# Optimization experiments

Hardware: AMD Instinct MI355X
Metric: run time of the kernel (lower is better)

The kernel has to match this reference:

```python
import jax, jax.numpy as jnp
import numpy as np

B, H, W, K = 256, 28, 28, 5

def grid_edges_np(nb, h, w):
    # directed 8-neighbor edges on an h x w grid, replicated for nb graphs
    idx = np.arange(h * w).reshape(h, w)
    src_l, dst_l = [], []
    for dy in (-1, 0, 1):
        for dx in (-1, 0, 1):
            if dy == 0 and dx == 0:
                continue
            s = idx[max(0, -dy):h - max(0, dy), max(0, -dx):w - max(0, dx)]
            d = idx[max(0, dy):h - max(0, -dy), max(0, dx):w - max(0, -dx)]
            src_l.append(s.ravel()); dst_l.append(d.ravel())
    e = np.stack([np.concatenate(src_l), np.concatenate(dst_l)])
    off = np.arange(nb) * h * w
    return (e[:, None, :] + off[None, :, None]).reshape(2, -1).astype(np.int32)

def cart_pseudo(pos, src, dst):
    # CartesianAdj: relative offsets normalized into [0,1]^2
    cart = pos[dst] - pos[src]
    return cart / (2.0 * jnp.max(jnp.abs(cart))) + 0.5

def spline_conv(x, src, dst, pseudo, Wk, root, bias):
    # SplineConv, dim=2, kernel_size=K, degree-1 open B-splines, mean aggregation
    n = x.shape[0]
    v = jnp.clip(pseudo, 0.0, 1.0) * (K - 1)
    i0 = jnp.clip(jnp.floor(v), 0, K - 1).astype(jnp.int32)
    frac = v - i0.astype(v.dtype)
    i1 = jnp.minimum(i0 + 1, K - 1)
    Y = jnp.einsum('nf,kfg->nkg', x, Wk)  # [N, K*K, Fout]
    msg = 0.0
    for ia, ba in ((i0[:, 0], 1.0 - frac[:, 0]), (i1[:, 0], frac[:, 0])):
        for jb, bb in ((i0[:, 1], 1.0 - frac[:, 1]), (i1[:, 1], frac[:, 1])):
            msg = msg + (ba * bb)[:, None] * Y[src, ia * K + jb]
    cnt = jax.ops.segment_sum(jnp.ones((src.shape[0],), x.dtype), dst, num_segments=n)
    agg = jax.ops.segment_sum(msg, dst, num_segments=n) / jnp.maximum(cnt, 1.0)[:, None]
    return agg + x @ root + bias

def voxel_pool(x, pos, size, gy, gx, npi):
    # voxel-grid clustering: max-pool features, mean-pool positions
    batch = jnp.repeat(jnp.arange(B), npi)
    c = jnp.floor(pos / size).astype(jnp.int32)
    c = jnp.clip(c, 0, jnp.array([gx - 1, gy - 1], dtype=jnp.int32))
    cid = batch * (gy * gx) + c[:, 1] * gx + c[:, 0]
    ns = B * gy * gx
    xp = jax.ops.segment_max(x, cid, num_segments=ns)
    cnt = jax.ops.segment_sum(jnp.ones((x.shape[0],), x.dtype), cid, num_segments=ns)
    pp = jax.ops.segment_sum(pos, cid, num_segments=ns) / cnt[:, None]
    return xp, pp

def setup_inputs():
    key = jax.random.key(0)
    ks = jax.random.split(key, 10)
    ei = grid_edges_np(B, H, W)
    yy, xx = np.meshgrid(np.arange(H), np.arange(W), indexing='ij')
    p = np.stack([xx.ravel(), yy.ravel()], 1).astype(np.float32)
    pos = np.tile(p, (B, 1))
    cart = pos[ei[1]] - pos[ei[0]]
    pseudo = (cart / (2.0 * np.abs(cart).max()) + 0.5).astype(np.float32)
    r = lambda k, s, sc: jax.random.normal(k, s, dtype=jnp.float32) * sc
    return {
        'x': jax.random.normal(ks[0], (B * H * W, 1), dtype=jnp.float32),
        'pos': jnp.asarray(pos), 'pseudo': jnp.asarray(pseudo),
        'W1': r(ks[1], (K * K, 1, 32), 0.3), 'root1': r(ks[2], (1, 32), 0.3), 'b1': jnp.zeros((32,), jnp.float32),
        'W2': r(ks[3], (K * K, 32, 64), 0.08), 'root2': r(ks[4], (32, 64), 0.08), 'b2': jnp.zeros((64,), jnp.float32),
        'W3': r(ks[5], (K * K, 64, 64), 0.06), 'root3': r(ks[6], (64, 64), 0.06), 'b3': jnp.zeros((64,), jnp.float32),
        'fc1_w': r(ks[7], (256, 128), 0.06), 'fc1_b': jnp.zeros((128,), jnp.float32),
        'fc2_w': r(ks[8], (128, 10), 0.09), 'fc2_b': jnp.zeros((10,), jnp.float32),
        'edge_index': jnp.asarray(ei),
    }

def reference(x, pos, pseudo, W1, root1, b1, W2, root2, b2, W3, root3, b3, fc1_w, fc1_b, fc2_w, fc2_b, edge_index):
    src, dst = edge_index[0], edge_index[1]
    h = jax.nn.elu(spline_conv(x, src, dst, pseudo, W1, root1, b1))
    h, pos1 = voxel_pool(h, pos, 5.0, 6, 6, H * W)            # 28x28 -> 6x6
    e1 = jnp.asarray(grid_edges_np(B, 6, 6))
    h = jax.nn.elu(spline_conv(h, e1[0], e1[1], cart_pseudo(pos1, e1[0], e1[1]), W2, root2, b2))
    h, pos2 = voxel_pool(h, pos1, 7.0, 4, 4, 36)              # 6x6 -> 4x4
    e2 = jnp.asarray(grid_edges_np(B, 4, 4))
    h = jax.nn.elu(spline_conv(h, e2[0], e2[1], cart_pseudo(pos2, e2[0], e2[1]), W3, root3, b3))
    h, _ = voxel_pool(h, pos2, 14.0, 2, 2, 16)                # dense pool -> 2x2 = 4 clusters
    h = h.reshape(B, 4 * 64)
    h = jax.nn.elu(h @ fc1_w + fc1_b)
    # dropout is identity in eval mode
    h = h @ fc2_w + fc2_b
    return jax.nn.log_softmax(h, axis=1)
```

## Files before the change

kernel.cpp:

```cpp
#include <hip/hip_runtime.h>
#include <hip/hip_bf16.h>
#include <math.h>


#define DEV __device__ __forceinline__

DEV float elu_f(float v) { return v > 0.f ? v : expm1f(v); }

DEV void corners(float p0, float p1,
                 int& k00, int& k01, int& k10, int& k11,
                 float& w00, float& w01, float& w10, float& w11) {
  float v0 = fminf(fmaxf(p0, 0.f), 1.f) * 4.f;
  float v1 = fminf(fmaxf(p1, 0.f), 1.f) * 4.f;
  int i0 = (int)v0; i0 = i0 > 4 ? 4 : i0;
  int j0 = (int)v1; j0 = j0 > 4 ? 4 : j0;
  float f0 = v0 - (float)i0;
  float f1 = v1 - (float)j0;
  int i1 = i0 + 1 > 4 ? 4 : i0 + 1;
  int j1 = j0 + 1 > 4 ? 4 : j0 + 1;
  k00 = i0 * 5 + j0; k01 = i0 * 5 + j1; k10 = i1 * 5 + j0; k11 = i1 * 5 + j1;
  w00 = (1.f - f0) * (1.f - f1); w01 = (1.f - f0) * f1;
  w10 = f0 * (1.f - f1);         w11 = f0 * f1;
}

DEV float cellpos(int c, int gw) {
  return (gw == 6) ? (c < 5 ? 2.f + 5.f * (float)c : 26.f)
                   : (c < 3 ? 2.f + 7.5f * (float)c : 24.f);
}

__constant__ int c_dys[8] = {-1, -1, -1, 0, 0, 1, 1, 1};
__constant__ int c_dxs[8] = {-1, 0, 1, -1, 1, -1, 0, 1};

__global__ __launch_bounds__(256) void s1p1_kernel(
    const float* __restrict__ xin, const float* __restrict__ W1,
    const float* __restrict__ root1, const float* __restrict__ b1,
    float* __restrict__ h1p) {
  int id = blockIdx.x * 256 + threadIdx.x;
  int g = id & 31, cell = id >> 5;
  int b = cell / 36, r = cell % 36;
  int cy = r / 6, cx = r % 6;
  int y0 = cy * 5, y1 = y0 + 5 > 28 ? 28 : y0 + 5;
  int x0 = cx * 5, x1 = x0 + 5 > 28 ? 28 : x0 + 5;
  float Wreg[8];
#pragma unroll
  for (int d = 0; d < 8; d++) {
    int k = (2 * c_dxs[d] + 2) * 5 + (2 * c_dys[d] + 2);
    Wreg[d] = W1[k * 32 + g];
  }
  float rt = root1[g], bs = b1[g];
  const float* xb = xin + b * 784;
  float vmax = -3.4e38f;
  for (int y = y0; y < y1; y++) {
    for (int x = x0; x < x1; x++) {
      float acc = 0.f;
#pragma unroll
      for (int d = 0; d < 8; d++) {
        int sy = y - c_dys[d], sx = x - c_dxs[d];
        if (sy >= 0 && sy < 28 && sx >= 0 && sx < 28)
          acc += xb[sy * 28 + sx] * Wreg[d];
      }
      float cnt = (float)((1 + (y > 0) + (y < 27)) * (1 + (x > 0) + (x < 27)) - 1);
      float v = acc * (1.f / cnt) + xb[y * 28 + x] * rt + bs;
      vmax = fmaxf(vmax, elu_f(v));
    }
  }
  h1p[cell * 32 + g] = vmax;
}

__global__ __launch_bounds__(256) void prepM_kernel(
    const float* __restrict__ W2, const float* __restrict__ root2,
    const float* __restrict__ W3, const float* __restrict__ root3,
    float* __restrict__ M2, float* __restrict__ M3) {
  int idx = blockIdx.x * 256 + threadIdx.x;
  const int L2N = 36 * 9 * 32 * 64;
  int gw, F, c, d, f, g;
  const float *W, *root;
  float inv2M;
  float* Mout;
  int oidx;
  if (idx < L2N) {
    c = idx / 18432; int rem = idx % 18432;
    d = rem / 2048; f = (rem >> 6) & 31; g = rem & 63;
    gw = 6; F = 32; W = W2; root = root2; inv2M = 0.1f; Mout = M2; oidx = idx;
  } else {
    int j = idx - L2N;
    c = j / 36864; int rem = j % 36864;
    d = rem / 4096; f = (rem >> 6) & 63; g = rem & 63;
    gw = 4; F = 64; W = W3; root = root3; inv2M = 1.f / 15.f; Mout = M3; oidx = j;
  }
  float val = 0.f;
  if (d == 8) {
    val = root[f * 64 + g];
  } else {
    int cy = c / gw, cx = c % gw;
    int sy = cy - c_dys[d], sx = cx - c_dxs[d];
    if (sy >= 0 && sy < gw && sx >= 0 && sx < gw) {
      int cnt = (1 + (cy > 0) + (cy < gw - 1)) * (1 + (cx > 0) + (cx < gw - 1)) - 1;
      float invc = 1.f / (float)cnt;
      float p0 = (cellpos(cx, gw) - cellpos(sx, gw)) * inv2M + 0.5f;
      float p1 = (cellpos(cy, gw) - cellpos(sy, gw)) * inv2M + 0.5f;
      int k00, k01, k10, k11; float w00, w01, w10, w11;
      corners(p0, p1, k00, k01, k10, k11, w00, w01, w10, w11);
      val = invc * (w00 * W[(k00 * F + f) * 64 + g] + w01 * W[(k01 * F + f) * 64 + g] +
                    w10 * W[(k10 * F + f) * 64 + g] + w11 * W[(k11 * F + f) * 64 + g]);
    }
  }
  Mout[oidx] = val;
}

__global__ __launch_bounds__(256) void gemm_cls_kernel(
    const float* __restrict__ X, const float* __restrict__ M,
    float* __restrict__ P, int per, int fshift, int NC, int dps, int gw) {
  __shared__ float At[16][64];
  __shared__ float Bt[16][64];
  __shared__ int nbL[9];
  int t = threadIdx.x;
  int b0 = blockIdx.x * 64, c = blockIdx.y, s = blockIdx.z;
  int F = 1 << fshift, fmask = F - 1;
  if (t < 9) {
    int cy = c / gw, cx = c % gw;
    int nb = c;
    if (t < 8) {
      int sy = cy - c_dys[t], sx = cx - c_dxs[t];
      nb = (sy >= 0 && sy < gw && sx >= 0 && sx < gw) ? sy * gw + sx : c;
    }
    nbL[t] = nb;
  }
  __syncthreads();

  int tx = t & 15, ty = t >> 4;
  int kqA = (t & 3) * 4, rA = t >> 2;
  int bkB = t >> 4, bnB = (t & 15) * 4;
  float acc[4][4];
#pragma unroll
  for (int i = 0; i < 4; i++)
#pragma unroll
    for (int j = 0; j < 4; j++) acc[i][j] = 0.f;

  int chunkK = dps << fshift;
  for (int k0 = 0; k0 < chunkK; k0 += 16) {
    int kA = k0 + kqA;
    int dA = s * dps + (kA >> fshift);
    int fA = kA & fmask;
    float4 xv = *(const float4*)&X[(((b0 + rA) * per + nbL[dA]) << fshift) + fA];
    int kB = k0 + bkB;
    int dB = s * dps + (kB >> fshift);
    int fB = kB & fmask;
    float4 bv = *(const float4*)&M[(size_t)(((c * 9 + dB) << fshift) + fB) * 64 + bnB];
    __syncthreads();
    At[kqA + 0][rA] = xv.x; At[kqA + 1][rA] = xv.y;
    At[kqA + 2][rA] = xv.z; At[kqA + 3][rA] = xv.w;
    *(float4*)&Bt[bkB][bnB] = bv;
    __syncthreads();
#pragma unroll
    for (int kk = 0; kk < 16; kk++) {
      float4 a = *(const float4*)&At[kk][ty * 4];
      float4 bb = *(const float4*)&Bt[kk][tx * 4];
      acc[0][0] += a.x * bb.x; acc[0][1] += a.x * bb.y; acc[0][2] += a.x * bb.z; acc[0][3] += a.x * bb.w;
      acc[1][0] += a.y * bb.x; acc[1][1] += a.y * bb.y; acc[1][2] += a.y * bb.z; acc[1][3] += a.y * bb.w;
      acc[2][0] += a.z * bb.x; acc[2][1] += a.z * bb.y; acc[2][2] += a.z * bb.z; acc[2][3] += a.z * bb.w;
      acc[3][0] += a.w * bb.x; acc[3][1] += a.w * bb.y; acc[3][2] += a.w * bb.z; acc[3][3] += a.w * bb.w;
    }
  }
  float* Pq = P + ((size_t)(s * NC + c) * 256 + b0) * 64;
#pragma unroll
  for (int i = 0; i < 4; i++) {
    float4 v = {acc[i][0], acc[i][1], acc[i][2], acc[i][3]};
    *(float4*)&Pq[(size_t)(ty * 4 + i) * 64 + tx * 4] = v;
  }
}

__global__ __launch_bounds__(256) void redpool2_kernel(
    const float* __restrict__ P, const float* __restrict__ bias,
    float* __restrict__ h2p) {
  int id = blockIdx.x * 256 + threadIdx.x;
  int g = id & 63, s2 = id >> 6;
  int b = s2 >> 4, r = s2 & 15;
  int oy = r >> 2, ox = r & 3;
  int ys = oy == 0 ? 0 : (oy == 1 ? 1 : (oy == 2 ? 3 : 4));
  int yn = (oy == 1 || oy == 3) ? 2 : 1;
  int xs = ox == 0 ? 0 : (ox == 1 ? 1 : (ox == 2 ? 3 : 4));
  int xn = (ox == 1 || ox == 3) ? 2 : 1;
  float bg = bias[g];
  const size_t CS = (size_t)36 * 256 * 64;
  float vmax = -3.4e38f;
  for (int yy = ys; yy < ys + yn; yy++)
    for (int xx = xs; xx < xs + xn; xx++) {
      size_t e = (size_t)((yy * 6 + xx) * 256 + b) * 64 + g;
      float v = P[e] + P[CS + e] + P[2 * CS + e] + bg;
      vmax = fmaxf(vmax, elu_f(v));
    }
  h2p[(size_t)s2 * 64 + g] = vmax;
}

__global__ __launch_bounds__(256) void redpool3_kernel(
    const float* __restrict__ P, const float* __restrict__ bias,
    float* __restrict__ h3p) {
  int id = blockIdx.x * 256 + threadIdx.x;
  int g = id & 63, s2 = id >> 6;
  int b = s2 >> 2, r = s2 & 3;
  int oy = r >> 1, ox = r & 1;
  float bg = bias[g];
  const size_t CS = (size_t)16 * 256 * 64;
  float vmax = -3.4e38f;
#pragma unroll
  for (int i = 0; i < 2; i++)
#pragma unroll
    for (int j = 0; j < 2; j++) {
      int cy = oy * 2 + i, cx = ox * 2 + j;
      size_t e = (size_t)((cy * 4 + cx) * 256 + b) * 64 + g;
      float v = bg;
#pragma unroll
      for (int q = 0; q < 9; q++) v += P[q * CS + e];
      vmax = fmaxf(vmax, elu_f(v));
    }
  h3p[(size_t)s2 * 64 + g] = vmax;
}

__global__ __launch_bounds__(128) void fc_head_kernel(
    const float* __restrict__ h3p, const float* __restrict__ fc1w,
    const float* __restrict__ fc1b, const float* __restrict__ fc2w,
    const float* __restrict__ fc2b, float* __restrict__ out) {
  __shared__ float Al[256];
  __shared__ float h4l[128];
  __shared__ float lg[10];
  int b = blockIdx.x, t = threadIdx.x;
  Al[t] = h3p[b * 256 + t];
  Al[t + 128] = h3p[b * 256 + 128 + t];
  __syncthreads();
  float acc = fc1b[t];
  for (int k = 0; k < 256; k++) acc += Al[k] * fc1w[k * 128 + t];
  h4l[t] = elu_f(acc);
  __syncthreads();
  if (t < 10) {
    float l = fc2b[t];
    for (int k = 0; k < 128; k++) l += h4l[k] * fc2w[k * 10 + t];
    lg[t] = l;
  }
  __syncthreads();
  if (t < 10) {
    float m = lg[0];
#pragma unroll
    for (int j = 1; j < 10; j++) m = fmaxf(m, lg[j]);
    float ssum = 0.f;
#pragma unroll
    for (int j = 0; j < 10; j++) ssum += expf(lg[j] - m);
    out[b * 10 + t] = lg[t] - m - logf(ssum);
  }
}

extern "C" void kernel_launch(void* const* d_in, const int* in_sizes, int n_in,
                              void* d_out, int out_size, void* d_ws, size_t ws_size,
                              hipStream_t stream) {
  const float* x     = (const float*)d_in[0];
  const float* W1    = (const float*)d_in[3];
  const float* root1 = (const float*)d_in[4];
  const float* b1    = (const float*)d_in[5];
  const float* W2    = (const float*)d_in[6];
  const float* root2 = (const float*)d_in[7];
  const float* b2    = (const float*)d_in[8];
  const float* W3    = (const float*)d_in[9];
  const float* root3 = (const float*)d_in[10];
  const float* b3    = (const float*)d_in[11];
  const float* fc1w  = (const float*)d_in[12];
  const float* fc1b  = (const float*)d_in[13];
  const float* fc2w  = (const float*)d_in[14];
  const float* fc2b  = (const float*)d_in[15];
  float* out = (float*)d_out;

  float* ws = (float*)d_ws;
  size_t o = 0;
  float* w_h1p = ws + o; o += (size_t)9216 * 32;
  float* w_M2  = ws + o; o += (size_t)36 * 9 * 32 * 64;
  float* w_M3  = ws + o; o += (size_t)16 * 9 * 64 * 64;
  float* w_P   = ws + o; o += (size_t)9 * 16 * 256 * 64;
  float* w_h2p = ws + o; o += (size_t)4096 * 64;
  float* w_h3p = ws + o; o += (size_t)1024 * 64;

  s1p1_kernel<<<1152, 256, 0, stream>>>(x, W1, root1, b1, w_h1p);
  prepM_kernel<<<4896, 256, 0, stream>>>(W2, root2, W3, root3, w_M2, w_M3);
  gemm_cls_kernel<<<dim3(4, 36, 3), 256, 0, stream>>>(w_h1p, w_M2, w_P, 36, 5, 36, 3, 6);
  redpool2_kernel<<<1024, 256, 0, stream>>>(w_P, b2, w_h2p);
  gemm_cls_kernel<<<dim3(4, 16, 9), 256, 0, stream>>>(w_h2p, w_M3, w_P, 16, 6, 16, 1, 4);
  redpool3_kernel<<<256, 256, 0, stream>>>(w_P, b3, w_h3p);
  fc_head_kernel<<<256, 128, 0, stream>>>(w_h3p, fc1w, fc1b, fc2w, fc2b, out);
}
```

Before: 176.0 us.

## Fuse whole network into one cooperative persistent kernel with grid syncs

Replaces the chain of seven kernel launches with one cooperative persistent kernel. Each stage runs as a grid-stride loop over virtual blocks, with grid.sync between stages, to remove launch gaps and per-kernel tail effects. The layer-3 reduce, pool and FC head are fused into one body, the fc1 dot product is split across 256 threads, and the GEMM parameters become template constants. The persistent grid is capped at 512 blocks, so stages with more blocks run serially. The grid-wide barriers add sync overhead in exchange.

```diff
diff --git a/kernel.cpp b/kernel.cpp
--- a/kernel.cpp
+++ b/kernel.cpp
@@ -1,6 +1,8 @@
 #include <hip/hip_runtime.h>
-#include <hip/hip_bf16.h>
+#include <hip/hip_cooperative_groups.h>
 #include <math.h>
+
+namespace cg = cooperative_groups;
 
 
 #define DEV __device__ __forceinline__
@@ -31,11 +33,16 @@
 __constant__ int c_dys[8] = {-1, -1, -1, 0, 0, 1, 1, 1};
 __constant__ int c_dxs[8] = {-1, 0, 1, -1, 1, -1, 0, 1};
 
-__global__ __launch_bounds__(256) void s1p1_kernel(
-    const float* __restrict__ xin, const float* __restrict__ W1,
-    const float* __restrict__ root1, const float* __restrict__ b1,
-    float* __restrict__ h1p) {
-  int id = blockIdx.x * 256 + threadIdx.x;
+union SMem {
+  struct { float At[16][64]; float Bt[16][64]; int nbL[9]; } g;
+  struct { float h3[16][64]; float Al[256]; float part[256];
+           float h4[128]; float lg[10]; } f;
+};
+
+
+DEV void s1p1_body(int id, const float* __restrict__ xin,
+                   const float* __restrict__ W1, const float* __restrict__ root1,
+                   const float* __restrict__ b1, float* __restrict__ h1p) {
   int g = id & 31, cell = id >> 5;
   int b = cell / 36, r = cell % 36;
   int cy = r / 6, cx = r % 6;
@@ -67,11 +74,10 @@
   h1p[cell * 32 + g] = vmax;
 }
 
-__global__ __launch_bounds__(256) void prepM_kernel(
-    const float* __restrict__ W2, const float* __restrict__ root2,
-    const float* __restrict__ W3, const float* __restrict__ root3,
-    float* __restrict__ M2, float* __restrict__ M3) {
-  int idx = blockIdx.x * 256 + threadIdx.x;
+DEV void prepM_body(int idx, const float* __restrict__ W2,
+                    const float* __restrict__ root2, const float* __restrict__ W3,
+                    const float* __restrict__ root3, float* __restrict__ M2,
+                    float* __restrict__ M3) {
   const int L2N = 36 * 9 * 32 * 64;
   int gw, F, c, d, f, g;
   const float *W, *root;
@@ -108,23 +114,22 @@
   Mout[oidx] = val;
 }
 
-__global__ __launch_bounds__(256) void gemm_cls_kernel(
-    const float* __restrict__ X, const float* __restrict__ M,
-    float* __restrict__ P, int per, int fshift, int NC, int dps, int gw) {
-  __shared__ float At[16][64];
-  __shared__ float Bt[16][64];
-  __shared__ int nbL[9];
-  int t = threadIdx.x;
-  int b0 = blockIdx.x * 64, c = blockIdx.y, s = blockIdx.z;
-  int F = 1 << fshift, fmask = F - 1;
+template <int PER, int FSHIFT, int NC, int DPS, int GW>
+DEV void gemm_body(int vb, int t, SMem* sm, const float* __restrict__ X,
+                   const float* __restrict__ M, float* __restrict__ P) {
+  int s = vb / (4 * NC);
+  int rem = vb - s * 4 * NC;
+  int c = rem >> 2;
+  int b0 = (rem & 3) * 64;
+  constexpr int F = 1 << FSHIFT, fmask = F - 1;
   if (t < 9) {
-    int cy = c / gw, cx = c % gw;
-    int nb = c;
+    int cy = c / GW, cx = c % GW;
+    int nbv = c;
     if (t < 8) {
       int sy = cy - c_dys[t], sx = cx - c_dxs[t];
-      nb = (sy >= 0 && sy < gw && sx >= 0 && sx < gw) ? sy * gw + sx : c;
-    }
-    nbL[t] = nb;
+      nbv = (sy >= 0 && sy < GW && sx >= 0 && sx < GW) ? sy * GW + sx : c;
+    }
+    sm->g.nbL[t] = nbv;
   }
   __syncthreads();
 
@@ -137,25 +142,25 @@
 #pragma unroll
     for (int j = 0; j < 4; j++) acc[i][j] = 0.f;
 
-  int chunkK = dps << fshift;
+  constexpr int chunkK = DPS << FSHIFT;
   for (int k0 = 0; k0 < chunkK; k0 += 16) {
     int kA = k0 + kqA;
-    int dA = s * dps + (kA >> fshift);
+    int dA = s * DPS + (kA >> FSHIFT);
     int fA = kA & fmask;
-    float4 xv = *(const float4*)&X[(((b0 + rA) * per + nbL[dA]) << fshift) + fA];
+    float4 xv = *(const float4*)&X[(((b0 + rA) * PER + sm->g.nbL[dA]) << FSHIFT) + fA];
     int kB = k0 + bkB;
-    int dB = s * dps + (kB >> fshift);
+    int dB = s * DPS + (kB >> FSHIFT);
     int fB = kB & fmask;
-    float4 bv = *(const float4*)&M[(size_t)(((c * 9 + dB) << fshift) + fB) * 64 + bnB];
+    float4 bv = *(const float4*)&M[(size_t)(((c * 9 + dB) << FSHIFT) + fB) * 64 + bnB];
     __syncthreads();
-    At[kqA + 0][rA] = xv.x; At[kqA + 1][rA] = xv.y;
-    At[kqA + 2][rA] = xv.z; At[kqA + 3][rA] = xv.w;
-    *(float4*)&Bt[bkB][bnB] = bv;
+    sm->g.At[kqA + 0][rA] = xv.x; sm->g.At[kqA + 1][rA] = xv.y;
+    sm->g.At[kqA + 2][rA] = xv.z; sm->g.At[kqA + 3][rA] = xv.w;
+    *(float4*)&sm->g.Bt[bkB][bnB] = bv;
     __syncthreads();
 #pragma unroll
     for (int kk = 0; kk < 16; kk++) {
-      float4 a = *(const float4*)&At[kk][ty * 4];
-      float4 bb = *(const float4*)&Bt[kk][tx * 4];
+      float4 a = *(const float4*)&sm->g.At[kk][ty * 4];
+      float4 bb = *(const float4*)&sm->g.Bt[kk][tx * 4];
       acc[0][0] += a.x * bb.x; acc[0][1] += a.x * bb.y; acc[0][2] += a.x * bb.z; acc[0][3] += a.x * bb.w;
       acc[1][0] += a.y * bb.x; acc[1][1] += a.y * bb.y; acc[1][2] += a.y * bb.z; acc[1][3] += a.y * bb.w;
       acc[2][0] += a.z * bb.x; acc[2][1] += a.z * bb.y; acc[2][2] += a.z * bb.z; acc[2][3] += a.z * bb.w;
@@ -170,10 +175,8 @@
   }
 }
 
-__global__ __launch_bounds__(256) void redpool2_kernel(
-    const float* __restrict__ P, const float* __restrict__ bias,
-    float* __restrict__ h2p) {
-  int id = blockIdx.x * 256 + threadIdx.x;
+DEV void redpool2_body(int id, const float* __restrict__ P,
+                       const float* __restrict__ bias, float* __restrict__ h2p) {
   int g = id & 63, s2 = id >> 6;
   int b = s2 >> 4, r = s2 & 15;
   int oy = r >> 2, ox = r & 3;
@@ -193,60 +196,139 @@
   h2p[(size_t)s2 * 64 + g] = vmax;
 }
 
-__global__ __launch_bounds__(256) void redpool3_kernel(
-    const float* __restrict__ P, const float* __restrict__ bias,
-    float* __restrict__ h3p) {
-  int id = blockIdx.x * 256 + threadIdx.x;
-  int g = id & 63, s2 = id >> 6;
-  int b = s2 >> 2, r = s2 & 3;
-  int oy = r >> 1, ox = r & 1;
-  float bg = bias[g];
+DEV void fc_body(int b, int t, SMem* sm, const float* __restrict__ P,
+                 const float* __restrict__ b3, const float* __restrict__ fc1w,
+                 const float* __restrict__ fc1b, const float* __restrict__ fc2w,
+                 const float* __restrict__ fc2b, float* __restrict__ out) {
   const size_t CS = (size_t)16 * 256 * 64;
-  float vmax = -3.4e38f;
-#pragma unroll
-  for (int i = 0; i < 2; i++)
-#pragma unroll
-    for (int j = 0; j < 2; j++) {
-      int cy = oy * 2 + i, cx = ox * 2 + j;
-      size_t e = (size_t)((cy * 4 + cx) * 256 + b) * 64 + g;
-      float v = bg;
-#pragma unroll
-      for (int q = 0; q < 9; q++) v += P[q * CS + e];
-      vmax = fmaxf(vmax, elu_f(v));
-    }
-  h3p[(size_t)s2 * 64 + g] = vmax;
-}
-
-__global__ __launch_bounds__(128) void fc_head_kernel(
-    const float* __restrict__ h3p, const float* __restrict__ fc1w,
-    const float* __restrict__ fc1b, const float* __restrict__ fc2w,
-    const float* __restrict__ fc2b, float* __restrict__ out) {
-  __shared__ float Al[256];
-  __shared__ float h4l[128];
-  __shared__ float lg[10];
-  int b = blockIdx.x, t = threadIdx.x;
-  Al[t] = h3p[b * 256 + t];
-  Al[t + 128] = h3p[b * 256 + 128 + t];
-  __syncthreads();
-  float acc = fc1b[t];
-  for (int k = 0; k < 256; k++) acc += Al[k] * fc1w[k * 128 + t];
-  h4l[t] = elu_f(acc);
+#pragma unroll
+  for (int i = 0; i < 4; i++) {
+    int idx = i * 256 + t;
+    int cell = idx >> 6, g = idx & 63;
+    float v = b3[g];
+    size_t e = (size_t)(cell * 256 + b) * 64 + g;
+#pragma unroll
+    for (int q = 0; q < 9; q++) v += P[q * CS + e];
+    sm->f.h3[cell][g] = elu_f(v);
+  }
+  __syncthreads();
+  {
+    int r = t >> 6, g = t & 63;
+    int oy = r >> 1, ox = r & 1;
+    float m = -3.4e38f;
+#pragma unroll
+    for (int i = 0; i < 2; i++)
+#pragma unroll
+      for (int j = 0; j < 2; j++)
+        m = fmaxf(m, sm->f.h3[(oy * 2 + i) * 4 + (ox * 2 + j)][g]);
+    sm->f.Al[t] = m;
+  }
+  __syncthreads();
+  {
+    int o = t & 127, half = t >> 7;
+    float acc = 0.f;
+    const float* wcol = fc1w + o;
+#pragma unroll 8
+    for (int k = half * 128; k < half * 128 + 128; k++)
+      acc += sm->f.Al[k] * wcol[k * 128];
+    sm->f.part[t] = acc;
+  }
+  __syncthreads();
+  if (t < 128)
+    sm->f.h4[t] = elu_f(sm->f.part[t] + sm->f.part[t + 128] + fc1b[t]);
   __syncthreads();
   if (t < 10) {
     float l = fc2b[t];
-    for (int k = 0; k < 128; k++) l += h4l[k] * fc2w[k * 10 + t];
-    lg[t] = l;
+#pragma unroll 8
+    for (int k = 0; k < 128; k++) l += sm->f.h4[k] * fc2w[k * 10 + t];
+    sm->f.lg[t] = l;
   }
   __syncthreads();
   if (t < 10) {
-    float m = lg[0];
-#pragma unroll
-    for (int j = 1; j < 10; j++) m = fmaxf(m, lg[j]);
+    float m = sm->f.lg[0];
+#pragma unroll
+    for (int j = 1; j < 10; j++) m = fmaxf(m, sm->f.lg[j]);
     float ssum = 0.f;
 #pragma unroll
-    for (int j = 0; j < 10; j++) ssum += expf(lg[j] - m);
-    out[b * 10 + t] = lg[t] - m - logf(ssum);
-  }
+    for (int j = 0; j < 10; j++) ssum += expf(sm->f.lg[j] - m);
+    out[b * 10 + t] = sm->f.lg[t] - m - logf(ssum);
+  }
+}
+
+struct NetArgs {
+  const float *x, *W1, *root1, *b1;
+  const float *W2, *root2, *b2;
+  const float *W3, *root3, *b3;
+  const float *fc1w, *fc1b, *fc2w, *fc2b;
+  float *out;
+  float *h1p, *M2, *M3, *P, *h2p;
+};
+
+__global__ __launch_bounds__(256, 2) void net_kernel(NetArgs a) {
+  __shared__ SMem sm;
+  cg::grid_group grid = cg::this_grid();
+  const int t = threadIdx.x;
+  const int nblk = gridDim.x;
+
+  for (int vb = blockIdx.x; vb < 6048; vb += nblk) {
+    if (vb < 1152) s1p1_body(vb * 256 + t, a.x, a.W1, a.root1, a.b1, a.h1p);
+    else           prepM_body((vb - 1152) * 256 + t, a.W2, a.root2, a.W3, a.root3,
+                              a.M2, a.M3);
+  }
+  __threadfence();
+  grid.sync();
+  for (int vb = blockIdx.x; vb < 432; vb += nblk)
+    gemm_body<36, 5, 36, 3, 6>(vb, t, &sm, a.h1p, a.M2, a.P);
+  __threadfence();
+  grid.sync();
+  for (int vb = blockIdx.x; vb < 1024; vb += nblk)
+    redpool2_body(vb * 256 + t, a.P, a.b2, a.h2p);
+  __threadfence();
+  grid.sync();
+  for (int vb = blockIdx.x; vb < 576; vb += nblk)
+    gemm_body<16, 6, 16, 1, 4>(vb, t, &sm, a.h2p, a.M3, a.P);
+  __threadfence();
+  grid.sync();
+  for (int vb = blockIdx.x; vb < 256; vb += nblk)
+    fc_body(vb, t, &sm, a.P, a.b3, a.fc1w, a.fc1b, a.fc2w, a.fc2b, a.out);
+}
+
+__global__ __launch_bounds__(256) void s1p1_kernel(
+    const float* __restrict__ xin, const float* __restrict__ W1,
+    const float* __restrict__ root1, const float* __restrict__ b1,
+    float* __restrict__ h1p) {
+  s1p1_body(blockIdx.x * 256 + threadIdx.x, xin, W1, root1, b1, h1p);
+}
+
+__global__ __launch_bounds__(256) void prepM_kernel(
+    const float* __restrict__ W2, const float* __restrict__ root2,
+    const float* __restrict__ W3, const float* __restrict__ root3,
+    float* __restrict__ M2, float* __restrict__ M3) {
+  prepM_body(blockIdx.x * 256 + threadIdx.x, W2, root2, W3, root3, M2, M3);
+}
+
+template <int PER, int FSHIFT, int NC, int DPS, int GW>
+__global__ __launch_bounds__(256) void gemm_cls_tk(
+    const float* __restrict__ X, const float* __restrict__ M,
+    float* __restrict__ P) {
+  __shared__ SMem sm;
+  int vb = (blockIdx.z * NC + blockIdx.y) * 4 + blockIdx.x;
+  gemm_body<PER, FSHIFT, NC, DPS, GW>(vb, threadIdx.x, &sm, X, M, P);
+}
+
+__global__ __launch_bounds__(256) void redpool2_kernel(
+    const float* __restrict__ P, const float* __restrict__ bias,
+    float* __restrict__ h2p) {
+  redpool2_body(blockIdx.x * 256 + threadIdx.x, P, bias, h2p);
+}
+
+__global__ __launch_bounds__(256) void fc_fused_kernel(
+    const float* __restrict__ P, const float* __restrict__ b3,
+    const float* __restrict__ fc1w, const float* __restrict__ fc1b,
+    const float* __restrict__ fc2w, const float* __restrict__ fc2b,
+    float* __restrict__ out) {
+  __shared__ SMem sm;
+  fc_body(blockIdx.x, threadIdx.x, &sm, P, b3, fc1w, fc1b, fc2w, fc2b, out);
 }
 
 extern "C" void kernel_launch(void* const* d_in, const int* in_sizes, int n_in,
@@ -275,13 +357,36 @@
   float* w_M3  = ws + o; o += (size_t)16 * 9 * 64 * 64;
   float* w_P   = ws + o; o += (size_t)9 * 16 * 256 * 64;
   float* w_h2p = ws + o; o += (size_t)4096 * 64;
-  float* w_h3p = ws + o; o += (size_t)1024 * 64;
-
-  s1p1_kernel<<<1152, 256, 0, stream>>>(x, W1, root1, b1, w_h1p);
-  prepM_kernel<<<4896, 256, 0, stream>>>(W2, root2, W3, root3, w_M2, w_M3);
-  gemm_cls_kernel<<<dim3(4, 36, 3), 256, 0, stream>>>(w_h1p, w_M2, w_P, 36, 5, 36, 3, 6);
-  redpool2_kernel<<<1024, 256, 0, stream>>>(w_P, b2, w_h2p);
-  gemm_cls_kernel<<<dim3(4, 16, 9), 256, 0, stream>>>(w_h2p, w_M3, w_P, 16, 6, 16, 1, 4);
-  redpool3_kernel<<<256, 256, 0, stream>>>(w_P, b3, w_h3p);
-  fc_head_kernel<<<256, 128, 0, stream>>>(w_h3p, fc1w, fc1b, fc2w, fc2b, out);
-}
+
+  NetArgs a;
+  a.x = x; a.W1 = W1; a.root1 = root1; a.b1 = b1;
+  a.W2 = W2; a.root2 = root2; a.b2 = b2;
+  a.W3 = W3; a.root3 = root3; a.b3 = b3;
+  a.fc1w = fc1w; a.fc1b = fc1b; a.fc2w = fc2w; a.fc2b = fc2b;
+  a.out = out;
+  a.h1p = w_h1p; a.M2 = w_M2; a.M3 = w_M3; a.P = w_P; a.h2p = w_h2p;
+
+  static int s_grid = 0;
+  if (s_grid == 0) {
+    int perCU = 0;
+    if (hipOccupancyMaxActiveBlocksPerMultiprocessor(
+            &perCU, (const void*)net_kernel, 256, 0) != hipSuccess || perCU <= 0)
+      perCU = 2;
+    long g = (long)perCU * 256;
+    s_grid = (int)(g < 512 ? g : 512);
+  }
+
+  void* kargs[] = { (void*)&a };
+  hipError_t err = hipLaunchCooperativeKernel((const void*)net_kernel,
+                                              dim3(s_grid), dim3(256), kargs,
+                                              0, stream);
+  if (err != hipSuccess) {
+    (void)hipGetLastError();
+    s1p1_kernel<<<1152, 256, 0, stream>>>(x, W1, root1, b1, w_h1p);
+    prepM_kernel<<<4896, 256, 0, stream>>>(W2, root2, W3, root3, w_M2, w_M3);
+    gemm_cls_tk<36, 5, 36, 3, 6><<<dim3(4, 36, 3), 256, 0, stream>>>(w_h1p, w_M2, w_P);
+    redpool2_kernel<<<1024, 256, 0, stream>>>(w_P, b2, w_h2p);
+    gemm_cls_tk<16, 6, 16, 1, 4><<<dim3(4, 16, 9), 256, 0, stream>>>(w_h2p, w_M3, w_P);
+    fc_fused_kernel<<<256, 256, 0, stream>>>(w_P, b3, fc1w, fc1b, fc2w, fc2b, out);
+  }
+}
```

Measured after the change: 493.5 us. 2.8x slower.

## Fuse pooling into GEMM epilogues via atomic max and merge prep kernels

Applied to the files above, without the earlier changes.

Merges the layer-1 conv+pool kernel, the spline weight-matrix precompute and the zeroing of the pooled buffers into one launch. The split-K GEMMs with separate reduce/pool kernels are replaced by full-K GEMMs that max-pool straight into order-preserving uint buffers with atomicMax. Bias and ELU are applied later, when the pooled value is read. This works because ELU plus a per-channel bias is monotone, so it commutes with max. It cuts launches and the large partial-sum traffic, but the GEMMs now run with far fewer blocks (144 and 128) and serial K loops, which may reduce parallelism. The FC head is also split over 256 threads.

```diff
diff --git a/kernel.cpp b/kernel.cpp
--- a/kernel.cpp
+++ b/kernel.cpp
@@ -1,11 +1,19 @@
 #include <hip/hip_runtime.h>
-#include <hip/hip_bf16.h>
 #include <math.h>
 
 
 #define DEV __device__ __forceinline__
 
 DEV float elu_f(float v) { return v > 0.f ? v : expm1f(v); }
+
+DEV unsigned int fmap(float f) {
+  unsigned int b = __float_as_uint(f);
+  return (b & 0x80000000u) ? ~b : (b | 0x80000000u);
+}
+DEV float funmap(unsigned int u) {
+  unsigned int b = (u & 0x80000000u) ? (u & 0x7fffffffu) : ~u;
+  return __uint_as_float(b);
+}
 
 DEV void corners(float p0, float p1,
                  int& k00, int& k01, int& k10, int& k11,
@@ -28,14 +36,15 @@
                    : (c < 3 ? 2.f + 7.5f * (float)c : 24.f);
 }
 
+DEV int ymap6(int c) { return c == 0 ? 0 : (c <= 2 ? 1 : (c == 3 ? 2 : 3)); }
+
 __constant__ int c_dys[8] = {-1, -1, -1, 0, 0, 1, 1, 1};
 __constant__ int c_dxs[8] = {-1, 0, 1, -1, 1, -1, 0, 1};
 
-__global__ __launch_bounds__(256) void s1p1_kernel(
-    const float* __restrict__ xin, const float* __restrict__ W1,
-    const float* __restrict__ root1, const float* __restrict__ b1,
-    float* __restrict__ h1p) {
-  int id = blockIdx.x * 256 + threadIdx.x;
+
+DEV void s1p1_body(int id, const float* __restrict__ xin,
+                   const float* __restrict__ W1, const float* __restrict__ root1,
+                   const float* __restrict__ b1, float* __restrict__ h1p) {
   int g = id & 31, cell = id >> 5;
   int b = cell / 36, r = cell % 36;
   int cy = r / 6, cx = r % 6;
@@ -67,11 +76,10 @@
   h1p[cell * 32 + g] = vmax;
 }
 
-__global__ __launch_bounds__(256) void prepM_kernel(
-    const float* __restrict__ W2, const float* __restrict__ root2,
-    const float* __restrict__ W3, const float* __restrict__ root3,
-    float* __restrict__ M2, float* __restrict__ M3) {
-  int idx = blockIdx.x * 256 + threadIdx.x;
+DEV void prepM_body(int idx, const float* __restrict__ W2,
+                    const float* __restrict__ root2, const float* __restrict__ W3,
+                    const float* __restrict__ root3, float* __restrict__ M2,
+                    float* __restrict__ M3) {
   const int L2N = 36 * 9 * 32 * 64;
   int gw, F, c, d, f, g;
   const float *W, *root;
@@ -108,23 +116,42 @@
   Mout[oidx] = val;
 }
 
-__global__ __launch_bounds__(256) void gemm_cls_kernel(
-    const float* __restrict__ X, const float* __restrict__ M,
-    float* __restrict__ P, int per, int fshift, int NC, int dps, int gw) {
+__global__ __launch_bounds__(256) void prep_kernel(
+    const float* __restrict__ x, const float* __restrict__ W1,
+    const float* __restrict__ root1, const float* __restrict__ b1,
+    const float* __restrict__ W2, const float* __restrict__ root2,
+    const float* __restrict__ W3, const float* __restrict__ root3,
+    float* __restrict__ h1p, float* __restrict__ M2, float* __restrict__ M3,
+    unsigned int* __restrict__ h2raw, unsigned int* __restrict__ h3raw) {
+  int vb = blockIdx.x, t = threadIdx.x;
+  if (vb < 1152) {
+    s1p1_body(vb * 256 + t, x, W1, root1, b1, h1p);
+  } else if (vb < 6048) {
+    prepM_body((vb - 1152) * 256 + t, W2, root2, W3, root3, M2, M3);
+  } else {
+    int id = (vb - 6048) * 256 + t;
+    if (id < 262144) h2raw[id] = 0u;
+    else             h3raw[id - 262144] = 0u;
+  }
+}
+
+__global__ __launch_bounds__(256) void gemm2_kernel(
+    const float* __restrict__ X, const float* __restrict__ M2,
+    unsigned int* __restrict__ h2raw) {
   __shared__ float At[16][64];
   __shared__ float Bt[16][64];
   __shared__ int nbL[9];
   int t = threadIdx.x;
-  int b0 = blockIdx.x * 64, c = blockIdx.y, s = blockIdx.z;
-  int F = 1 << fshift, fmask = F - 1;
+  int c = blockIdx.x >> 2;
+  int b0 = (blockIdx.x & 3) * 64;
+  int cy = c / 6, cx = c % 6;
   if (t < 9) {
-    int cy = c / gw, cx = c % gw;
-    int nb = c;
+    int nbv = c;
     if (t < 8) {
       int sy = cy - c_dys[t], sx = cx - c_dxs[t];
-      nb = (sy >= 0 && sy < gw && sx >= 0 && sx < gw) ? sy * gw + sx : c;
-    }
-    nbL[t] = nb;
+      nbv = (sy >= 0 && sy < 6 && sx >= 0 && sx < 6) ? sy * 6 + sx : c;
+    }
+    nbL[t] = nbv;
   }
   __syncthreads();
 
@@ -137,16 +164,10 @@
 #pragma unroll
     for (int j = 0; j < 4; j++) acc[i][j] = 0.f;
 
-  int chunkK = dps << fshift;
-  for (int k0 = 0; k0 < chunkK; k0 += 16) {
-    int kA = k0 + kqA;
-    int dA = s * dps + (kA >> fshift);
-    int fA = kA & fmask;
-    float4 xv = *(const float4*)&X[(((b0 + rA) * per + nbL[dA]) << fshift) + fA];
-    int kB = k0 + bkB;
-    int dB = s * dps + (kB >> fshift);
-    int fB = kB & fmask;
-    float4 bv = *(const float4*)&M[(size_t)(((c * 9 + dB) << fshift) + fB) * 64 + bnB];
+  for (int k0 = 0; k0 < 288; k0 += 16) {
+    int d = k0 >> 5, fb = k0 & 31;
+    float4 xv = *(const float4*)&X[(((b0 + rA) * 36 + nbL[d]) << 5) + fb + kqA];
+    float4 bv = *(const float4*)&M2[(size_t)(((c * 9 + d) << 5) + fb + bkB) * 64 + bnB];
     __syncthreads();
     At[kqA + 0][rA] = xv.x; At[kqA + 1][rA] = xv.y;
     At[kqA + 2][rA] = xv.z; At[kqA + 3][rA] = xv.w;
@@ -162,79 +183,104 @@
       acc[3][0] += a.w * bb.x; acc[3][1] += a.w * bb.y; acc[3][2] += a.w * bb.z; acc[3][3] += a.w * bb.w;
     }
   }
-  float* Pq = P + ((size_t)(s * NC + c) * 256 + b0) * 64;
+  int r = ymap6(cy) * 4 + ymap6(cx);
 #pragma unroll
   for (int i = 0; i < 4; i++) {
-    float4 v = {acc[i][0], acc[i][1], acc[i][2], acc[i][3]};
-    *(float4*)&Pq[(size_t)(ty * 4 + i) * 64 + tx * 4] = v;
-  }
-}
-
-__global__ __launch_bounds__(256) void redpool2_kernel(
-    const float* __restrict__ P, const float* __restrict__ bias,
-    float* __restrict__ h2p) {
-  int id = blockIdx.x * 256 + threadIdx.x;
-  int g = id & 63, s2 = id >> 6;
-  int b = s2 >> 4, r = s2 & 15;
-  int oy = r >> 2, ox = r & 3;
-  int ys = oy == 0 ? 0 : (oy == 1 ? 1 : (oy == 2 ? 3 : 4));
-  int yn = (oy == 1 || oy == 3) ? 2 : 1;
-  int xs = ox == 0 ? 0 : (ox == 1 ? 1 : (ox == 2 ? 3 : 4));
-  int xn = (ox == 1 || ox == 3) ? 2 : 1;
-  float bg = bias[g];
-  const size_t CS = (size_t)36 * 256 * 64;
-  float vmax = -3.4e38f;
-  for (int yy = ys; yy < ys + yn; yy++)
-    for (int xx = xs; xx < xs + xn; xx++) {
-      size_t e = (size_t)((yy * 6 + xx) * 256 + b) * 64 + g;
-      float v = P[e] + P[CS + e] + P[2 * CS + e] + bg;
-      vmax = fmaxf(vmax, elu_f(v));
-    }
-  h2p[(size_t)s2 * 64 + g] = vmax;
-}
-
-__global__ __launch_bounds__(256) void redpool3_kernel(
-    const float* __restrict__ P, const float* __restrict__ bias,
-    float* __restrict__ h3p) {
-  int id = blockIdx.x * 256 + threadIdx.x;
-  int g = id & 63, s2 = id >> 6;
-  int b = s2 >> 2, r = s2 & 3;
-  int oy = r >> 1, ox = r & 1;
-  float bg = bias[g];
-  const size_t CS = (size_t)16 * 256 * 64;
-  float vmax = -3.4e38f;
+    int b = b0 + ty * 4 + i;
+    unsigned int* dst = &h2raw[(size_t)(b * 16 + r) * 64 + tx * 4];
+#pragma unroll
+    for (int j = 0; j < 4; j++) atomicMax(&dst[j], fmap(acc[i][j]));
+  }
+}
+
+__global__ __launch_bounds__(256) void gemm3_kernel(
+    const unsigned int* __restrict__ H2, const float* __restrict__ M3,
+    const float* __restrict__ b2, unsigned int* __restrict__ h3raw) {
+  __shared__ float At[16][32];
+  __shared__ float Bt[16][64];
+  __shared__ int nbL[9];
+  int t = threadIdx.x;
+  int c = blockIdx.x >> 3;
+  int b0 = (blockIdx.x & 7) * 32;
+  int cy = c >> 2, cx = c & 3;
+  if (t < 9) {
+    int nbv = c;
+    if (t < 8) {
+      int sy = cy - c_dys[t], sx = cx - c_dxs[t];
+      nbv = (sy >= 0 && sy < 4 && sx >= 0 && sx < 4) ? sy * 4 + sx : c;
+    }
+    nbL[t] = nbv;
+  }
+  __syncthreads();
+
+  int tx = t & 15, ty = t >> 4;
+  int rr = t >> 3, fo = (t & 7) * 2;
+  int bkB = t >> 4, bnB = (t & 15) * 4;
+  float acc[2][4];
 #pragma unroll
   for (int i = 0; i < 2; i++)
 #pragma unroll
-    for (int j = 0; j < 2; j++) {
-      int cy = oy * 2 + i, cx = ox * 2 + j;
-      size_t e = (size_t)((cy * 4 + cx) * 256 + b) * 64 + g;
-      float v = bg;
-#pragma unroll
-      for (int q = 0; q < 9; q++) v += P[q * CS + e];
-      vmax = fmaxf(vmax, elu_f(v));
-    }
-  h3p[(size_t)s2 * 64 + g] = vmax;
-}
-
-__global__ __launch_bounds__(128) void fc_head_kernel(
-    const float* __restrict__ h3p, const float* __restrict__ fc1w,
-    const float* __restrict__ fc1b, const float* __restrict__ fc2w,
-    const float* __restrict__ fc2b, float* __restrict__ out) {
+    for (int j = 0; j < 4; j++) acc[i][j] = 0.f;
+
+  for (int k0 = 0; k0 < 576; k0 += 16) {
+    int d = k0 >> 6, fb = (k0 & 63);
+    int f = fb + fo;
+    uint2 hv = *(const uint2*)&H2[(size_t)(((b0 + rr) * 16 + nbL[d]) << 6) + f];
+    float a0 = elu_f(funmap(hv.x) + b2[f]);
+    float a1 = elu_f(funmap(hv.y) + b2[f + 1]);
+    float4 bv = *(const float4*)&M3[(size_t)(((c * 9 + d) << 6) + fb + bkB) * 64 + bnB];
+    __syncthreads();
+    At[fo + 0][rr] = a0; At[fo + 1][rr] = a1;
+    *(float4*)&Bt[bkB][bnB] = bv;
+    __syncthreads();
+#pragma unroll
+    for (int kk = 0; kk < 16; kk++) {
+      float a0c = At[kk][ty * 2 + 0];
+      float a1c = At[kk][ty * 2 + 1];
+      float4 bb = *(const float4*)&Bt[kk][tx * 4];
+      acc[0][0] += a0c * bb.x; acc[0][1] += a0c * bb.y; acc[0][2] += a0c * bb.z; acc[0][3] += a0c * bb.w;
+      acc[1][0] += a1c * bb.x; acc[1][1] += a1c * bb.y; acc[1][2] += a1c * bb.z; acc[1][3] += a1c * bb.w;
+    }
+  }
+  int r = (cy >> 1) * 2 + (cx >> 1);
+#pragma unroll
+  for (int i = 0; i < 2; i++) {
+    int b = b0 + ty * 2 + i;
+    unsigned int* dst = &h3raw[(size_t)(b * 4 + r) * 64 + tx * 4];
+#pragma unroll
+    for (int j = 0; j < 4; j++) atomicMax(&dst[j], fmap(acc[i][j]));
+  }
+}
+
+__global__ __launch_bounds__(256) void fc_kernel(
+    const unsigned int* __restrict__ h3raw, const float* __restrict__ b3,
+    const float* __restrict__ fc1w, const float* __restrict__ fc1b,
+    const float* __restrict__ fc2w, const float* __restrict__ fc2b,
+    float* __restrict__ out) {
   __shared__ float Al[256];
-  __shared__ float h4l[128];
+  __shared__ float part[256];
+  __shared__ float h4[128];
   __shared__ float lg[10];
   int b = blockIdx.x, t = threadIdx.x;
-  Al[t] = h3p[b * 256 + t];
-  Al[t + 128] = h3p[b * 256 + 128 + t];
-  __syncthreads();
-  float acc = fc1b[t];
-  for (int k = 0; k < 256; k++) acc += Al[k] * fc1w[k * 128 + t];
-  h4l[t] = elu_f(acc);
+  Al[t] = elu_f(funmap(h3raw[b * 256 + t]) + b3[t & 63]);
+  __syncthreads();
+  {
+    int o = t & 127, half = t >> 7;
+    float acc = 0.f;
+    const float* wcol = fc1w + o;
+#pragma unroll 8
+    for (int k = half * 128; k < half * 128 + 128; k++)
+      acc += Al[k] * wcol[k * 128];
+    part[t] = acc;
+  }
+  __syncthreads();
+  if (t < 128)
+    h4[t] = elu_f(part[t] + part[t + 128] + fc1b[t]);
   __syncthreads();
   if (t < 10) {
     float l = fc2b[t];
-    for (int k = 0; k < 128; k++) l += h4l[k] * fc2w[k * 10 + t];
+#pragma unroll 8
+    for (int k = 0; k < 128; k++) l += h4[k] * fc2w[k * 10 + t];
     lg[t] = l;
   }
   __syncthreads();
@@ -273,15 +319,12 @@
   float* w_h1p = ws + o; o += (size_t)9216 * 32;
   float* w_M2  = ws + o; o += (size_t)36 * 9 * 32 * 64;
   float* w_M3  = ws + o; o += (size_t)16 * 9 * 64 * 64;
-  float* w_P   = ws + o; o += (size_t)9 * 16 * 256 * 64;
-  float* w_h2p = ws + o; o += (size_t)4096 * 64;
-  float* w_h3p = ws + o; o += (size_t)1024 * 64;
-
-  s1p1_kernel<<<1152, 256, 0, stream>>>(x, W1, root1, b1, w_h1p);
-  prepM_kernel<<<4896, 256, 0, stream>>>(W2, root2, W3, root3, w_M2, w_M3);
-  gemm_cls_kernel<<<dim3(4, 36, 3), 256, 0, stream>>>(w_h1p, w_M2, w_P, 36, 5, 36, 3, 6);
-  redpool2_kernel<<<1024, 256, 0, stream>>>(w_P, b2, w_h2p);
-  gemm_cls_kernel<<<dim3(4, 16, 9), 256, 0, stream>>>(w_h2p, w_M3, w_P, 16, 6, 16, 1, 4);
-  redpool3_kernel<<<256, 256, 0, stream>>>(w_P, b3, w_h3p);
-  fc_head_kernel<<<256, 128, 0, stream>>>(w_h3p, fc1w, fc1b, fc2w, fc2b, out);
-}
+  unsigned int* w_h2raw = (unsigned int*)(ws + o); o += 262144;
+  unsigned int* w_h3raw = (unsigned int*)(ws + o); o += 65536;
+
+  prep_kernel<<<7328, 256, 0, stream>>>(x, W1, root1, b1, W2, root2, W3, root3,
+                                        w_h1p, w_M2, w_M3, w_h2raw, w_h3raw);
+  gemm2_kernel<<<144, 256, 0, stream>>>(w_h1p, w_M2, w_h2raw);
+  gemm3_kernel<<<128, 256, 0, stream>>>(w_h2raw, w_M3, b2, w_h3raw);
+  fc_kernel<<<256, 256, 0, stream>>>(w_h3raw, b3, fc1w, fc1b, fc2w, fc2b, out);
+}
```

New measurement: 205.7 us. +16.8%, slower.

## Merge prep kernels, fuse layer-3 pooling into FC head, templatize GEMM

Applied to the files above, without the earlier changes.

Combines the layer-1 conv+pool and the M2/M3 weight-prep into a single launch, and folds the layer-3 reduce/pool into the FC head kernel, which now uses 256 threads with a split-K fc1. The grouped GEMM is templated so the shape parameters become compile-time constants, and the interior layer-1 pixels take a branch-free stencil path. The aim is fewer kernel launches, less intermediate global traffic and cheaper index arithmetic. In exchange the fused head adds shared memory and extra sync points per block.

```diff
diff --git a/kernel.cpp b/kernel.cpp
--- a/kernel.cpp
+++ b/kernel.cpp
@@ -1,5 +1,4 @@
 #include <hip/hip_runtime.h>
-#include <hip/hip_bf16.h>
 #include <math.h>
 
 
@@ -31,11 +30,10 @@
 __constant__ int c_dys[8] = {-1, -1, -1, 0, 0, 1, 1, 1};
 __constant__ int c_dxs[8] = {-1, 0, 1, -1, 1, -1, 0, 1};
 
-__global__ __launch_bounds__(256) void s1p1_kernel(
-    const float* __restrict__ xin, const float* __restrict__ W1,
-    const float* __restrict__ root1, const float* __restrict__ b1,
-    float* __restrict__ h1p) {
-  int id = blockIdx.x * 256 + threadIdx.x;
+
+DEV void s1p1_body(int id, const float* __restrict__ xin,
+                   const float* __restrict__ W1, const float* __restrict__ root1,
+                   const float* __restrict__ b1, float* __restrict__ h1p) {
   int g = id & 31, cell = id >> 5;
   int b = cell / 36, r = cell % 36;
   int cy = r / 6, cx = r % 6;
@@ -51,27 +49,36 @@
   const float* xb = xin + b * 784;
   float vmax = -3.4e38f;
   for (int y = y0; y < y1; y++) {
+    bool yin = (y > 0) && (y < 27);
     for (int x = x0; x < x1; x++) {
-      float acc = 0.f;
-#pragma unroll
-      for (int d = 0; d < 8; d++) {
-        int sy = y - c_dys[d], sx = x - c_dxs[d];
-        if (sy >= 0 && sy < 28 && sx >= 0 && sx < 28)
-          acc += xb[sy * 28 + sx] * Wreg[d];
+      float v;
+      if (yin && (x > 0) && (x < 27)) {
+        float acc = 0.f;
+#pragma unroll
+        for (int d = 0; d < 8; d++)
+          acc += xb[(y - c_dys[d]) * 28 + (x - c_dxs[d])] * Wreg[d];
+        v = acc * 0.125f + xb[y * 28 + x] * rt + bs;
+      } else {
+        float acc = 0.f;
+#pragma unroll
+        for (int d = 0; d < 8; d++) {
+          int sy = y - c_dys[d], sx = x - c_dxs[d];
+          if (sy >= 0 && sy < 28 && sx >= 0 && sx < 28)
+            acc += xb[sy * 28 + sx] * Wreg[d];
+        }
+        float cnt = (float)((1 + (y > 0) + (y < 27)) * (1 + (x > 0) + (x < 27)) - 1);
+        v = acc * (1.f / cnt) + xb[y * 28 + x] * rt + bs;
       }
-      float cnt = (float)((1 + (y > 0) + (y < 27)) * (1 + (x > 0) + (x < 27)) - 1);
-      float v = acc * (1.f / cnt) + xb[y * 28 + x] * rt + bs;
       vmax = fmaxf(vmax, elu_f(v));
     }
   }
   h1p[cell * 32 + g] = vmax;
 }
 
-__global__ __launch_bounds__(256) void prepM_kernel(
-    const float* __restrict__ W2, const float* __restrict__ root2,
-    const float* __restrict__ W3, const float* __restrict__ root3,
-    float* __restrict__ M2, float* __restrict__ M3) {
-  int idx = blockIdx.x * 256 + threadIdx.x;
+DEV void prepM_body(int idx, const float* __restrict__ W2,
+                    const float* __restrict__ root2, const float* __restrict__ W3,
+                    const float* __restrict__ root3, float* __restrict__ M2,
+                    float* __restrict__ M3) {
   const int L2N = 36 * 9 * 32 * 64;
   int gw, F, c, d, f, g;
   const float *W, *root;
@@ -108,23 +115,36 @@
   Mout[oidx] = val;
 }
 
-__global__ __launch_bounds__(256) void gemm_cls_kernel(
-    const float* __restrict__ X, const float* __restrict__ M,
-    float* __restrict__ P, int per, int fshift, int NC, int dps, int gw) {
+__global__ __launch_bounds__(256) void prep_kernel(
+    const float* __restrict__ x, const float* __restrict__ W1,
+    const float* __restrict__ root1, const float* __restrict__ b1,
+    const float* __restrict__ W2, const float* __restrict__ root2,
+    const float* __restrict__ W3, const float* __restrict__ root3,
+    float* __restrict__ h1p, float* __restrict__ M2, float* __restrict__ M3) {
+  int vb = blockIdx.x, t = threadIdx.x;
+  if (vb < 1152) s1p1_body(vb * 256 + t, x, W1, root1, b1, h1p);
+  else           prepM_body((vb - 1152) * 256 + t, W2, root2, W3, root3, M2, M3);
+}
+
+template <int PER, int FSHIFT, int NC, int DPS, int GW>
+DEV void gemm_body(int vb, int t, const float* __restrict__ X,
+                   const float* __restrict__ M, float* __restrict__ P) {
   __shared__ float At[16][64];
   __shared__ float Bt[16][64];
   __shared__ int nbL[9];
-  int t = threadIdx.x;
-  int b0 = blockIdx.x * 64, c = blockIdx.y, s = blockIdx.z;
-  int F = 1 << fshift, fmask = F - 1;
+  int s = vb / (4 * NC);
+  int rem = vb - s * 4 * NC;
+  int c = rem >> 2;
+  int b0 = (rem & 3) * 64;
+  constexpr int F = 1 << FSHIFT, fmask = F - 1;
   if (t < 9) {
-    int cy = c / gw, cx = c % gw;
-    int nb = c;
+    int cy = c / GW, cx = c % GW;
+    int nbv = c;
     if (t < 8) {
       int sy = cy - c_dys[t], sx = cx - c_dxs[t];
-      nb = (sy >= 0 && sy < gw && sx >= 0 && sx < gw) ? sy * gw + sx : c;
-    }
-    nbL[t] = nb;
+      nbv = (sy >= 0 && sy < GW && sx >= 0 && sx < GW) ? sy * GW + sx : c;
+    }
+    nbL[t] = nbv;
   }
   __syncthreads();
 
@@ -137,16 +157,16 @@
 #pragma unroll
     for (int j = 0; j < 4; j++) acc[i][j] = 0.f;
 
-  int chunkK = dps << fshift;
+  constexpr int chunkK = DPS << FSHIFT;
   for (int k0 = 0; k0 < chunkK; k0 += 16) {
     int kA = k0 + kqA;
-    int dA = s * dps + (kA >> fshift);
+    int dA = s * DPS + (kA >> FSHIFT);
     int fA = kA & fmask;
-    float4 xv = *(const float4*)&X[(((b0 + rA) * per + nbL[dA]) << fshift) + fA];
+    float4 xv = *(const float4*)&X[(((b0 + rA) * PER + nbL[dA]) << FSHIFT) + fA];
     int kB = k0 + bkB;
-    int dB = s * dps + (kB >> fshift);
+    int dB = s * DPS + (kB >> FSHIFT);
     int fB = kB & fmask;
-    float4 bv = *(const float4*)&M[(size_t)(((c * 9 + dB) << fshift) + fB) * 64 + bnB];
+    float4 bv = *(const float4*)&M[(size_t)(((c * 9 + dB) << FSHIFT) + fB) * 64 + bnB];
     __syncthreads();
     At[kqA + 0][rA] = xv.x; At[kqA + 1][rA] = xv.y;
     At[kqA + 2][rA] = xv.z; At[kqA + 3][rA] = xv.w;
@@ -168,6 +188,14 @@
     float4 v = {acc[i][0], acc[i][1], acc[i][2], acc[i][3]};
     *(float4*)&Pq[(size_t)(ty * 4 + i) * 64 + tx * 4] = v;
   }
+}
+
+template <int PER, int FSHIFT, int NC, int DPS, int GW>
+__global__ __launch_bounds__(256) void gemm_cls_tk(
+    const float* __restrict__ X, const float* __restrict__ M,
+    float* __restrict__ P) {
+  int vb = (blockIdx.z * NC + blockIdx.y) * 4 + blockIdx.x;
+  gemm_body<PER, FSHIFT, NC, DPS, GW>(vb, threadIdx.x, X, M, P);
 }
 
 __global__ __launch_bounds__(256) void redpool2_kernel(
@@ -193,48 +221,58 @@
   h2p[(size_t)s2 * 64 + g] = vmax;
 }
 
-__global__ __launch_bounds__(256) void redpool3_kernel(
-    const float* __restrict__ P, const float* __restrict__ bias,
-    float* __restrict__ h3p) {
-  int id = blockIdx.x * 256 + threadIdx.x;
-  int g = id & 63, s2 = id >> 6;
-  int b = s2 >> 2, r = s2 & 3;
-  int oy = r >> 1, ox = r & 1;
-  float bg = bias[g];
-  const size_t CS = (size_t)16 * 256 * 64;
-  float vmax = -3.4e38f;
-#pragma unroll
-  for (int i = 0; i < 2; i++)
-#pragma unroll
-    for (int j = 0; j < 2; j++) {
-      int cy = oy * 2 + i, cx = ox * 2 + j;
-      size_t e = (size_t)((cy * 4 + cx) * 256 + b) * 64 + g;
-      float v = bg;
-#pragma unroll
-      for (int q = 0; q < 9; q++) v += P[q * CS + e];
-      vmax = fmaxf(vmax, elu_f(v));
-    }
-  h3p[(size_t)s2 * 64 + g] = vmax;
-}
-
-__global__ __launch_bounds__(128) void fc_head_kernel(
-    const float* __restrict__ h3p, const float* __restrict__ fc1w,
-    const float* __restrict__ fc1b, const float* __restrict__ fc2w,
-    const float* __restrict__ fc2b, float* __restrict__ out) {
+__global__ __launch_bounds__(256) void fc_fused_kernel(
+    const float* __restrict__ P, const float* __restrict__ b3,
+    const float* __restrict__ fc1w, const float* __restrict__ fc1b,
+    const float* __restrict__ fc2w, const float* __restrict__ fc2b,
+    float* __restrict__ out) {
+  __shared__ float h3[16][64];
   __shared__ float Al[256];
-  __shared__ float h4l[128];
+  __shared__ float part[256];
+  __shared__ float h4[128];
   __shared__ float lg[10];
   int b = blockIdx.x, t = threadIdx.x;
-  Al[t] = h3p[b * 256 + t];
-  Al[t + 128] = h3p[b * 256 + 128 + t];
-  __syncthreads();
-  float acc = fc1b[t];
-  for (int k = 0; k < 256; k++) acc += Al[k] * fc1w[k * 128 + t];
-  h4l[t] = elu_f(acc);
+  const size_t CS = (size_t)16 * 256 * 64;
+#pragma unroll
+  for (int i = 0; i < 4; i++) {
+    int idx = i * 256 + t;
+    int cell = idx >> 6, g = idx & 63;
+    float v = b3[g];
+    size_t e = (size_t)(cell * 256 + b) * 64 + g;
+#pragma unroll
+    for (int q = 0; q < 9; q++) v += P[q * CS + e];
+    h3[cell][g] = elu_f(v);
+  }
+  __syncthreads();
+  {
+    int r = t >> 6, g = t & 63;
+    int oy = r >> 1, ox = r & 1;
+    float m = -3.4e38f;
+#pragma unroll
+    for (int i = 0; i < 2; i++)
+#pragma unroll
+      for (int j = 0; j < 2; j++)
+        m = fmaxf(m, h3[(oy * 2 + i) * 4 + (ox * 2 + j)][g]);
+    Al[t] = m;
+  }
+  __syncthreads();
+  {
+    int o = t & 127, half = t >> 7;
+    float acc = 0.f;
+    const float* wcol = fc1w + o;
+#pragma unroll 8
+    for (int k = half * 128; k < half * 128 + 128; k++)
+      acc += Al[k] * wcol[k * 128];
+    part[t] = acc;
+  }
+  __syncthreads();
+  if (t < 128)
+    h4[t] = elu_f(part[t] + part[t + 128] + fc1b[t]);
   __syncthreads();
   if (t < 10) {
     float l = fc2b[t];
-    for (int k = 0; k < 128; k++) l += h4l[k] * fc2w[k * 10 + t];
+#pragma unroll 8
+    for (int k = 0; k < 128; k++) l += h4[k] * fc2w[k * 10 + t];
     lg[t] = l;
   }
   __syncthreads();
@@ -275,13 +313,11 @@
   float* w_M3  = ws + o; o += (size_t)16 * 9 * 64 * 64;
   float* w_P   = ws + o; o += (size_t)9 * 16 * 256 * 64;
   float* w_h2p = ws + o; o += (size_t)4096 * 64;
-  float* w_h3p = ws + o; o += (size_t)1024 * 64;
-
-  s1p1_kernel<<<1152, 256, 0, stream>>>(x, W1, root1, b1, w_h1p);
-  prepM_kernel<<<4896, 256, 0, stream>>>(W2, root2, W3, root3, w_M2, w_M3);
-  gemm_cls_kernel<<<dim3(4, 36, 3), 256, 0, stream>>>(w_h1p, w_M2, w_P, 36, 5, 36, 3, 6);
+
+  prep_kernel<<<6048, 256, 0, stream>>>(x, W1, root1, b1, W2, root2, W3, root3,
+                                        w_h1p, w_M2, w_M3);
+  gemm_cls_tk<36, 5, 36, 3, 6><<<dim3(4, 36, 3), 256, 0, stream>>>(w_h1p, w_M2, w_P);
   redpool2_kernel<<<1024, 256, 0, stream>>>(w_P, b2, w_h2p);
-  gemm_cls_kernel<<<dim3(4, 16, 9), 256, 0, stream>>>(w_h2p, w_M3, w_P, 16, 6, 16, 1, 4);
-  redpool3_kernel<<<256, 256, 0, stream>>>(w_P, b3, w_h3p);
-  fc_head_kernel<<<256, 128, 0, stream>>>(w_h3p, fc1w, fc1b, fc2w, fc2b, out);
-}
+  gemm_cls_tk<16, 6, 16, 1, 4><<<dim3(4, 16, 9), 256, 0, stream>>>(w_h2p, w_M3, w_P);
+  fc_fused_kernel<<<256, 256, 0, stream>>>(w_P, b3, fc1w, fc1b, fc2w, fc2b, out);
+}
```

Result: faster. 162.1 us (-7.9%).
